# Kernel optimization log

Measured on AMD Instinct MI355X. Metric: run time of the kernel, lower is better.

The kernel has to match this reference:

```python
import jax, jax.numpy as jnp
import numpy as np

TAU = 0.2
NUM_SAMPLES = 8192
EMBED = 64


def setup_inputs() -> dict:
    key = jax.random.key(0)
    k1, k2, k3, k4 = jax.random.split(key, 4)
    all_users = jax.random.normal(k1, (100000, EMBED), dtype=jnp.float32)
    all_items = jax.random.normal(k2, (50000, EMBED), dtype=jnp.float32)
    user_index = jax.random.randint(k3, (NUM_SAMPLES,), 0, 100000, dtype=jnp.int64 if jax.config.jax_enable_x64 else jnp.int32)
    item_index = jax.random.randint(k4, (NUM_SAMPLES,), 0, 50000, dtype=jnp.int64 if jax.config.jax_enable_x64 else jnp.int32)
    return {"all_users": all_users, "all_items": all_items,
            "user_index": user_index, "item_index": item_index}


def _ssm_loss(embed, tau):
    # ratings: [N, N] similarity; positive is the diagonal (self-similarity).
    ratings = jnp.matmul(embed, embed.T) / tau            # [N, N]
    diag = jnp.sum(embed * embed, axis=1) / tau           # diag of embed@embed.T, no NxN gather
    # -log( exp(diag) / sum_j exp(ratings_ij) ) = logsumexp_row - diag
    lse = jax.scipy.special.logsumexp(ratings, axis=1)    # [N]
    return jnp.mean(lse - diag)


def reference(all_users, all_items, user_index, item_index):
    selected_users = all_users[user_index]                # [N, d]
    selected_items = all_items[item_index]                # [N, d]
    loss_u = _ssm_loss(selected_users, TAU)
    loss_i = _ssm_loss(selected_items, TAU)
    inv_loss = loss_u + loss_i
    return inv_loss, jnp.stack([loss_u, loss_i])
```

## Files before the change

kernel.cpp:

```cpp
#include <hip/hip_runtime.h>

#define EMBED        64
#define NS           8192
#define NTILE        256
#define JCHUNKS      8
#define JT_PER_CHUNK 32
#define C_L2E_TAU    7.21347520444482f

typedef _Float16 half8  __attribute__((ext_vector_type(8)));
typedef float    f32x16 __attribute__((ext_vector_type(16)));

static __device__ __forceinline__ float exp2_raw(float x) {
  float r;
  asm("v_exp_f32 %0, %1" : "=v"(r) : "v"(x));
  return r;
}

__global__ __launch_bounds__(256) void prep_kernel(
    const float* __restrict__ users, const float* __restrict__ items,
    const int* __restrict__ uidx, const int* __restrict__ iidx,
    _Float16* __restrict__ Efrag, float* __restrict__ diag) {
  int b = blockIdx.x;
  int mat = b >> 8, tile = b & 255;
  int kt = threadIdx.x >> 6;
  int lane = threadIdx.x & 63;
  int r = lane & 31;
  int k0 = kt * 16 + (lane >> 5) * 8;
  int row = tile * 32 + r;
  int src = mat ? iidx[row] : uidx[row];
  const float4* basep =
      (const float4*)((mat ? items : users) + (size_t)src * EMBED + k0);
  float4 v0 = basep[0], v1 = basep[1];
  float vs[8] = {v0.x, v0.y, v0.z, v0.w, v1.x, v1.y, v1.z, v1.w};

  half8 hh, ll;
  float p = 0.f;
  #pragma unroll
  for (int j = 0; j < 8; ++j) {
    float v = vs[j];
    _Float16 h = (_Float16)v;
    hh[j] = h;
    ll[j] = (_Float16)(v - (float)h);
    p = fmaf(v, v, p);
  }
  _Float16* tb = Efrag + (size_t)(mat * NTILE + tile) * 4096;
  *(half8*)(tb + ((kt)     * 64 + lane) * 8) = hh;
  *(half8*)(tb + ((4 + kt) * 64 + lane) * 8) = ll;

  p += __shfl_xor(p, 32);
  __shared__ float ds[4][32];
  if (lane < 32) ds[kt][lane] = p;
  __syncthreads();
  if (threadIdx.x < 32)
    diag[mat * NS + tile * 32 + threadIdx.x] =
        ds[0][threadIdx.x] + ds[1][threadIdx.x] +
        ds[2][threadIdx.x] + ds[3][threadIdx.x];
}

__global__ __launch_bounds__(256, 4) void ssm_mfma_kernel(
    const _Float16* __restrict__ Efrag, const float* __restrict__ diag,
    float* __restrict__ rowpart) {
  int b = blockIdx.x;
  int jc  = b & (JCHUNKS - 1);
  int sg  = (b >> 3) & 63;
  int mat = b >> 9;
  int wave = threadIdx.x >> 6;
  int lane = threadIdx.x & 63;
  int hf   = lane >> 5;

  int rowtile = sg * 4 + wave;
  const _Float16* Em = Efrag + (size_t)mat * NTILE * 4096;

  half8 a[8];
  #pragma unroll
  for (int f = 0; f < 8; ++f)
    a[f] = *(const half8*)(Em + (size_t)rowtile * 4096 + (f * 64 + lane) * 8);

  float negdv[16];
  #pragma unroll
  for (int r = 0; r < 16; ++r)
    negdv[r] = -diag[mat * NS + rowtile * 32 + (r & 3) + 8 * (r >> 2) + 4 * hf];

  float rs[16];
  #pragma unroll
  for (int r = 0; r < 16; ++r) rs[r] = 0.f;

  int tj0 = jc * JT_PER_CHUNK;

  #pragma unroll 2
  for (int jt = 0; jt < JT_PER_CHUNK; ++jt) {
    const _Float16* B = Em + (size_t)(tj0 + jt) * 4096;
    half8 bh[4], bl[4];
    #pragma unroll
    for (int k = 0; k < 4; ++k)
      bh[k] = *(const half8*)(B + ((k)     * 64 + lane) * 8);
    #pragma unroll
    for (int k = 0; k < 4; ++k)
      bl[k] = *(const half8*)(B + ((4 + k) * 64 + lane) * 8);

    f32x16 acc;
    #pragma unroll
    for (int r = 0; r < 16; ++r) acc[r] = negdv[r];

    #pragma unroll
    for (int k = 0; k < 4; ++k)
      acc = __builtin_amdgcn_mfma_f32_32x32x16_f16(a[k], bh[k], acc, 0, 0, 0);
    #pragma unroll
    for (int k = 0; k < 4; ++k)
      acc = __builtin_amdgcn_mfma_f32_32x32x16_f16(a[k], bl[k], acc, 0, 0, 0);
    #pragma unroll
    for (int k = 0; k < 4; ++k)
      acc = __builtin_amdgcn_mfma_f32_32x32x16_f16(a[4 + k], bh[k], acc, 0, 0, 0);

    #pragma unroll
    for (int r = 0; r < 16; ++r)
      rs[r] += exp2_raw(acc[r] * C_L2E_TAU);
  }

  #pragma unroll
  for (int r = 0; r < 16; ++r) {
    float v = rs[r];
    #pragma unroll
    for (int off = 16; off; off >>= 1) v += __shfl_xor(v, off);
    if ((lane & 31) == 0)
      rowpart[jc * (2 * NS) + mat * NS + rowtile * 32 +
              (r & 3) + 8 * (r >> 2) + 4 * hf] = v;
  }
}

__global__ __launch_bounds__(1024) void finalize_kernel(
    const float* __restrict__ rowpart, float* __restrict__ out) {
  float lu = 0.f, li = 0.f;
  for (int r = threadIdx.x; r < 2 * NS; r += 1024) {
    float s = 0.f;
    #pragma unroll
    for (int c = 0; c < JCHUNKS; ++c) s += rowpart[c * (2 * NS) + r];
    float l = logf(s);
    if (r < NS) lu += l; else li += l;
  }
  #pragma unroll
  for (int off = 32; off; off >>= 1) {
    lu += __shfl_down(lu, off);
    li += __shfl_down(li, off);
  }
  __shared__ float red[2][16];
  int wave = threadIdx.x >> 6;
  if ((threadIdx.x & 63) == 0) { red[0][wave] = lu; red[1][wave] = li; }
  __syncthreads();
  if (threadIdx.x == 0) {
    float su = 0.f, si = 0.f;
    #pragma unroll
    for (int w = 0; w < 16; ++w) { su += red[0][w]; si += red[1][w]; }
    su *= (1.0f / NS);
    si *= (1.0f / NS);
    out[0] = su + si;
    out[1] = su;
    out[2] = si;
  }
}

extern "C" void kernel_launch(void* const* d_in, const int* in_sizes, int n_in,
                              void* d_out, int out_size, void* d_ws, size_t ws_size,
                              hipStream_t stream) {
  const float* users = (const float*)d_in[0];
  const float* items = (const float*)d_in[1];
  const int*   uidx  = (const int*)d_in[2];
  const int*   iidx  = (const int*)d_in[3];
  float* out = (float*)d_out;

  _Float16* Efrag = (_Float16*)d_ws;
  float* diag     = (float*)((char*)d_ws + (size_t)4194304);
  float* rowpart  = diag + 2 * NS;

  prep_kernel<<<2 * NTILE, 256, 0, stream>>>(users, items, uidx, iidx, Efrag, diag);
  ssm_mfma_kernel<<<2 * 64 * JCHUNKS, 256, 0, stream>>>(Efrag, diag, rowpart);
  finalize_kernel<<<1, 1024, 0, stream>>>(rowpart, out);
}
```

Measured before the change: 146.3 us.

## Double-buffer B tile loads and split MFMA chain into independent accumulators

Restructures the j-loop into a software-pipelined double buffer, prefetching the next B tile into registers while the current tile runs through its MFMAs. The single dependent 12-MFMA chain becomes three independent accumulator chains that are summed afterwards, which shortens the dependency latency. The diagonal offset is pre-scaled and folded into a single fma before exp2. Launch bounds are relaxed from 4 to 2 blocks per CU to make room for the extra registers, which may lower occupancy.

```diff
diff --git a/kernel.cpp b/kernel.cpp
--- a/kernel.cpp
+++ b/kernel.cpp
@@ -57,7 +57,7 @@
         ds[2][threadIdx.x] + ds[3][threadIdx.x];
 }
 
-__global__ __launch_bounds__(256, 4) void ssm_mfma_kernel(
+__global__ __launch_bounds__(256, 2) void ssm_mfma_kernel(
     const _Float16* __restrict__ Efrag, const float* __restrict__ diag,
     float* __restrict__ rowpart) {
   int b = blockIdx.x;
@@ -76,10 +76,11 @@
   for (int f = 0; f < 8; ++f)
     a[f] = *(const half8*)(Em + (size_t)rowtile * 4096 + (f * 64 + lane) * 8);
 
-  float negdv[16];
+  float negdvC[16];
   #pragma unroll
   for (int r = 0; r < 16; ++r)
-    negdv[r] = -diag[mat * NS + rowtile * 32 + (r & 3) + 8 * (r >> 2) + 4 * hf];
+    negdvC[r] = -diag[mat * NS + rowtile * 32 +
+                      (r & 3) + 8 * (r >> 2) + 4 * hf] * C_L2E_TAU;
 
   float rs[16];
   #pragma unroll
@@ -87,34 +88,37 @@
 
   int tj0 = jc * JT_PER_CHUNK;
 
-  #pragma unroll 2
-  for (int jt = 0; jt < JT_PER_CHUNK; ++jt) {
-    const _Float16* B = Em + (size_t)(tj0 + jt) * 4096;
-    half8 bh[4], bl[4];
+  auto loadB = [&](int tj, half8* bb) {
+    const _Float16* B = Em + (size_t)tj * 4096;
     #pragma unroll
-    for (int k = 0; k < 4; ++k)
-      bh[k] = *(const half8*)(B + ((k)     * 64 + lane) * 8);
+    for (int f = 0; f < 8; ++f)
+      bb[f] = *(const half8*)(B + (f * 64 + lane) * 8);
+  };
+
+  auto compute = [&](const half8* bb) {
+    f32x16 c0 = {0.f,0.f,0.f,0.f,0.f,0.f,0.f,0.f,
+                 0.f,0.f,0.f,0.f,0.f,0.f,0.f,0.f};
+    f32x16 c1 = c0, c2 = c0;
     #pragma unroll
-    for (int k = 0; k < 4; ++k)
-      bl[k] = *(const half8*)(B + ((4 + k) * 64 + lane) * 8);
-
-    f32x16 acc;
-    #pragma unroll
-    for (int r = 0; r < 16; ++r) acc[r] = negdv[r];
-
-    #pragma unroll
-    for (int k = 0; k < 4; ++k)
-      acc = __builtin_amdgcn_mfma_f32_32x32x16_f16(a[k], bh[k], acc, 0, 0, 0);
-    #pragma unroll
-    for (int k = 0; k < 4; ++k)
-      acc = __builtin_amdgcn_mfma_f32_32x32x16_f16(a[k], bl[k], acc, 0, 0, 0);
-    #pragma unroll
-    for (int k = 0; k < 4; ++k)
-      acc = __builtin_amdgcn_mfma_f32_32x32x16_f16(a[4 + k], bh[k], acc, 0, 0, 0);
-
+    for (int k = 0; k < 4; ++k) {
+      c0 = __builtin_amdgcn_mfma_f32_32x32x16_f16(a[k],     bb[k],     c0, 0, 0, 0);
+      c1 = __builtin_amdgcn_mfma_f32_32x32x16_f16(a[k],     bb[4 + k], c1, 0, 0, 0);
+      c2 = __builtin_amdgcn_mfma_f32_32x32x16_f16(a[4 + k], bb[k],     c2, 0, 0, 0);
+    }
+    f32x16 s = (c0 + c1) + c2;
     #pragma unroll
     for (int r = 0; r < 16; ++r)
-      rs[r] += exp2_raw(acc[r] * C_L2E_TAU);
+      rs[r] += exp2_raw(fmaf(s[r], C_L2E_TAU, negdvC[r]));
+  };
+
+  half8 bA[8], bB[8];
+  loadB(tj0, bA);
+  #pragma unroll 1
+  for (int jt = 0; jt < JT_PER_CHUNK; jt += 2) {
+    loadB(tj0 + jt + 1, bB);
+    compute(bA);
+    if (jt + 2 < JT_PER_CHUNK) loadB(tj0 + jt + 2, bA);
+    compute(bB);
   }
 
   #pragma unroll
```

Result: no change. 148.6 us (+1.6%).

## Stage B tiles through LDS with async double-buffering and fuse finalize via atomic ticket

Applied to the files above, without the earlier changes.

The main kernel now copies pairs of B tiles into a double-buffered LDS area using global_load_lds, so the next pair loads while the current one is computed. All four waves in a block then share each B tile from LDS instead of each fetching it from global memory. The three MFMA chains now use separate accumulators so they can run independently. The separate finalize launch is removed: the last block to finish, picked by an atomic counter, does the log-sum reduction itself. This saves a kernel launch but adds block-wide syncs and 32 KB of LDS per block, which may reduce occupancy.

```diff
diff --git a/kernel.cpp b/kernel.cpp
--- a/kernel.cpp
+++ b/kernel.cpp
@@ -5,10 +5,16 @@
 #define NTILE        256
 #define JCHUNKS      8
 #define JT_PER_CHUNK 32
+#define NPHASE       (JT_PER_CHUNK / 2)
+#define NBLOCKS_MAIN (2 * 64 * JCHUNKS)
 #define C_L2E_TAU    7.21347520444482f
 
 typedef _Float16 half8  __attribute__((ext_vector_type(8)));
 typedef float    f32x16 __attribute__((ext_vector_type(16)));
+
+#define GLDS16(g, l) __builtin_amdgcn_global_load_lds( \
+    (const __attribute__((address_space(1))) void*)(g), \
+    (__attribute__((address_space(3))) void*)(l), 16, 0, 0)
 
 static __device__ __forceinline__ float exp2_raw(float x) {
   float r;
@@ -19,8 +25,10 @@
 __global__ __launch_bounds__(256) void prep_kernel(
     const float* __restrict__ users, const float* __restrict__ items,
     const int* __restrict__ uidx, const int* __restrict__ iidx,
-    _Float16* __restrict__ Efrag, float* __restrict__ diag) {
+    _Float16* __restrict__ Efrag, float* __restrict__ diag,
+    int* __restrict__ done_cnt) {
   int b = blockIdx.x;
+  if (b == 0 && threadIdx.x == 0) *done_cnt = 0;
   int mat = b >> 8, tile = b & 255;
   int kt = threadIdx.x >> 6;
   int lane = threadIdx.x & 63;
@@ -59,7 +67,8 @@
 
 __global__ __launch_bounds__(256, 4) void ssm_mfma_kernel(
     const _Float16* __restrict__ Efrag, const float* __restrict__ diag,
-    float* __restrict__ rowpart) {
+    float* __restrict__ rowpart, int* __restrict__ done_cnt,
+    float* __restrict__ out) {
   int b = blockIdx.x;
   int jc  = b & (JCHUNKS - 1);
   int sg  = (b >> 3) & 63;
@@ -85,36 +94,45 @@
   #pragma unroll
   for (int r = 0; r < 16; ++r) rs[r] = 0.f;
 
+  __shared__ __align__(16) _Float16 Bbuf[2][8192];
+
   int tj0 = jc * JT_PER_CHUNK;
-
-  #pragma unroll 2
-  for (int jt = 0; jt < JT_PER_CHUNK; ++jt) {
-    const _Float16* B = Em + (size_t)(tj0 + jt) * 4096;
-    half8 bh[4], bl[4];
-    #pragma unroll
-    for (int k = 0; k < 4; ++k)
-      bh[k] = *(const half8*)(B + ((k)     * 64 + lane) * 8);
-    #pragma unroll
-    for (int k = 0; k < 4; ++k)
-      bl[k] = *(const half8*)(B + ((4 + k) * 64 + lane) * 8);
-
-    f32x16 acc;
-    #pragma unroll
-    for (int r = 0; r < 16; ++r) acc[r] = negdv[r];
-
-    #pragma unroll
-    for (int k = 0; k < 4; ++k)
-      acc = __builtin_amdgcn_mfma_f32_32x32x16_f16(a[k], bh[k], acc, 0, 0, 0);
-    #pragma unroll
-    for (int k = 0; k < 4; ++k)
-      acc = __builtin_amdgcn_mfma_f32_32x32x16_f16(a[k], bl[k], acc, 0, 0, 0);
-    #pragma unroll
-    for (int k = 0; k < 4; ++k)
-      acc = __builtin_amdgcn_mfma_f32_32x32x16_f16(a[4 + k], bh[k], acc, 0, 0, 0);
-
+  auto stage = [&](int buf, int pair) {
+    const char* src = (const char*)(Em + (size_t)(tj0 + 2 * pair) * 4096);
+    char* dst = (char*)&Bbuf[buf][0];
+    int o = wave * 4096;
+    #pragma unroll
+    for (int q = 0; q < 4; ++q)
+      GLDS16(src + o + q * 1024 + lane * 16, dst + o + q * 1024);
+  };
+
+  auto compute = [&](const _Float16* B) {
+    f32x16 c0, c1, c2;
+    #pragma unroll
+    for (int r = 0; r < 16; ++r) { c0[r] = negdv[r]; c1[r] = 0.f; c2[r] = 0.f; }
+    #pragma unroll
+    for (int k = 0; k < 4; ++k) {
+      half8 bh = *(const half8*)(B + ((k)     * 64 + lane) * 8);
+      half8 bl = *(const half8*)(B + ((4 + k) * 64 + lane) * 8);
+      c0 = __builtin_amdgcn_mfma_f32_32x32x16_f16(a[k],     bh, c0, 0, 0, 0);
+      c1 = __builtin_amdgcn_mfma_f32_32x32x16_f16(a[k],     bl, c1, 0, 0, 0);
+      c2 = __builtin_amdgcn_mfma_f32_32x32x16_f16(a[4 + k], bh, c2, 0, 0, 0);
+    }
+    f32x16 s = (c0 + c1) + c2;
     #pragma unroll
     for (int r = 0; r < 16; ++r)
-      rs[r] += exp2_raw(acc[r] * C_L2E_TAU);
+      rs[r] += exp2_raw(s[r] * C_L2E_TAU);
+  };
+
+  stage(0, 0);
+  __syncthreads();
+
+  for (int p = 0; p < NPHASE; ++p) {
+    if (p + 1 < NPHASE) stage((p + 1) & 1, p + 1);
+    const _Float16* B = &Bbuf[p & 1][0];
+    compute(B);
+    compute(B + 4096);
+    __syncthreads();
   }
 
   #pragma unroll
@@ -126,36 +144,39 @@
       rowpart[jc * (2 * NS) + mat * NS + rowtile * 32 +
               (r & 3) + 8 * (r >> 2) + 4 * hf] = v;
   }
-}
-
-__global__ __launch_bounds__(1024) void finalize_kernel(
-    const float* __restrict__ rowpart, float* __restrict__ out) {
-  float lu = 0.f, li = 0.f;
-  for (int r = threadIdx.x; r < 2 * NS; r += 1024) {
-    float s = 0.f;
-    #pragma unroll
-    for (int c = 0; c < JCHUNKS; ++c) s += rowpart[c * (2 * NS) + r];
-    float l = logf(s);
-    if (r < NS) lu += l; else li += l;
-  }
-  #pragma unroll
-  for (int off = 32; off; off >>= 1) {
-    lu += __shfl_down(lu, off);
-    li += __shfl_down(li, off);
-  }
-  __shared__ float red[2][16];
-  int wave = threadIdx.x >> 6;
-  if ((threadIdx.x & 63) == 0) { red[0][wave] = lu; red[1][wave] = li; }
+
+  __shared__ int sticket;
+  __threadfence();
+  if (threadIdx.x == 0) sticket = atomicAdd(done_cnt, 1);
   __syncthreads();
-  if (threadIdx.x == 0) {
-    float su = 0.f, si = 0.f;
-    #pragma unroll
-    for (int w = 0; w < 16; ++w) { su += red[0][w]; si += red[1][w]; }
-    su *= (1.0f / NS);
-    si *= (1.0f / NS);
-    out[0] = su + si;
-    out[1] = su;
-    out[2] = si;
+  if (sticket == NBLOCKS_MAIN - 1) {
+    __threadfence();
+    float lu = 0.f, li = 0.f;
+    for (int r = threadIdx.x; r < 2 * NS; r += 256) {
+      float s = 0.f;
+      #pragma unroll
+      for (int c = 0; c < JCHUNKS; ++c) s += rowpart[c * (2 * NS) + r];
+      float l = logf(s);
+      if (r < NS) lu += l; else li += l;
+    }
+    #pragma unroll
+    for (int off = 32; off; off >>= 1) {
+      lu += __shfl_down(lu, off);
+      li += __shfl_down(li, off);
+    }
+    __shared__ float red[2][4];
+    if ((threadIdx.x & 63) == 0) {
+      red[0][threadIdx.x >> 6] = lu;
+      red[1][threadIdx.x >> 6] = li;
+    }
+    __syncthreads();
+    if (threadIdx.x == 0) {
+      float su = (red[0][0] + red[0][1] + red[0][2] + red[0][3]) * (1.0f / NS);
+      float si = (red[1][0] + red[1][1] + red[1][2] + red[1][3]) * (1.0f / NS);
+      out[0] = su + si;
+      out[1] = su;
+      out[2] = si;
+    }
   }
 }
 
@@ -171,8 +192,10 @@
   _Float16* Efrag = (_Float16*)d_ws;
   float* diag     = (float*)((char*)d_ws + (size_t)4194304);
   float* rowpart  = diag + 2 * NS;
-
-  prep_kernel<<<2 * NTILE, 256, 0, stream>>>(users, items, uidx, iidx, Efrag, diag);
-  ssm_mfma_kernel<<<2 * 64 * JCHUNKS, 256, 0, stream>>>(Efrag, diag, rowpart);
-  finalize_kernel<<<1, 1024, 0, stream>>>(rowpart, out);
-}
+  int* done_cnt   = (int*)(rowpart + JCHUNKS * 2 * NS);
+
+  prep_kernel<<<2 * NTILE, 256, 0, stream>>>(users, items, uidx, iidx,
+                                             Efrag, diag, done_cnt);
+  ssm_mfma_kernel<<<NBLOCKS_MAIN, 256, 0, stream>>>(Efrag, diag, rowpart,
+                                                    done_cnt, out);
+}
```

New measurement: 281.1 us. 92.2% more time.

## Exploit Gram matrix symmetry to compute only upper-triangle tiles with atomics

Applied to the files above, without the earlier changes.

Because embed@embed.T is symmetric, each 32x32 tile above the diagonal is now computed once. Its exp values are added both to the row sums and, through column sums and atomicAdd, to the transposed rows. This removes about half of the MFMA and exp work. B tiles are now staged into double-buffered LDS with global_load_lds, the grid is reorganised into 16 j-chunks with early exit for blocks below the diagonal, and per-chunk partial buffers are replaced by a single atomic accumulator zeroed in prep. The cost is more exp work per tile, atomic contention, load imbalance across blocks, and nondeterministic float summation order.

```diff
diff --git a/kernel.cpp b/kernel.cpp
--- a/kernel.cpp
+++ b/kernel.cpp
@@ -3,12 +3,16 @@
 #define EMBED        64
 #define NS           8192
 #define NTILE        256
-#define JCHUNKS      8
-#define JT_PER_CHUNK 32
+#define NJC          16
+#define JT_PER_CHUNK 16
 #define C_L2E_TAU    7.21347520444482f
 
 typedef _Float16 half8  __attribute__((ext_vector_type(8)));
 typedef float    f32x16 __attribute__((ext_vector_type(16)));
+
+#define GLDS16(g, l) __builtin_amdgcn_global_load_lds( \
+    (const __attribute__((address_space(1))) void*)(g), \
+    (__attribute__((address_space(3))) void*)(l), 16, 0, 0)
 
 static __device__ __forceinline__ float exp2_raw(float x) {
   float r;
@@ -19,9 +23,11 @@
 __global__ __launch_bounds__(256) void prep_kernel(
     const float* __restrict__ users, const float* __restrict__ items,
     const int* __restrict__ uidx, const int* __restrict__ iidx,
-    _Float16* __restrict__ Efrag, float* __restrict__ diag) {
+    _Float16* __restrict__ Efrag, float* __restrict__ diag,
+    float* __restrict__ accum) {
   int b = blockIdx.x;
   int mat = b >> 8, tile = b & 255;
+  if (threadIdx.x < 32) accum[mat * NS + tile * 32 + threadIdx.x] = 0.f;
   int kt = threadIdx.x >> 6;
   int lane = threadIdx.x & 63;
   int r = lane & 31;
@@ -57,64 +63,91 @@
         ds[2][threadIdx.x] + ds[3][threadIdx.x];
 }
 
-__global__ __launch_bounds__(256, 4) void ssm_mfma_kernel(
+__global__ __launch_bounds__(256) void ssm_mfma_kernel(
     const _Float16* __restrict__ Efrag, const float* __restrict__ diag,
-    float* __restrict__ rowpart) {
+    float* __restrict__ accum) {
   int b = blockIdx.x;
-  int jc  = b & (JCHUNKS - 1);
-  int sg  = (b >> 3) & 63;
-  int mat = b >> 9;
+  int jc  = b & (NJC - 1);
+  int ig  = (b >> 4) & 63;
+  int mat = b >> 10;
+  if (jc * 16 + 15 < ig * 4) return;
+
   int wave = threadIdx.x >> 6;
   int lane = threadIdx.x & 63;
   int hf   = lane >> 5;
-
-  int rowtile = sg * 4 + wave;
+  int myI  = ig * 4 + wave;
   const _Float16* Em = Efrag + (size_t)mat * NTILE * 4096;
 
   half8 a[8];
   #pragma unroll
   for (int f = 0; f < 8; ++f)
-    a[f] = *(const half8*)(Em + (size_t)rowtile * 4096 + (f * 64 + lane) * 8);
-
-  float negdv[16];
+    a[f] = *(const half8*)(Em + (size_t)myI * 4096 + (f * 64 + lane) * 8);
+
+  float negdIC[16];
   #pragma unroll
   for (int r = 0; r < 16; ++r)
-    negdv[r] = -diag[mat * NS + rowtile * 32 + (r & 3) + 8 * (r >> 2) + 4 * hf];
+    negdIC[r] = -diag[mat * NS + myI * 32 +
+                      (r & 3) + 8 * (r >> 2) + 4 * hf] * C_L2E_TAU;
 
   float rs[16];
   #pragma unroll
   for (int r = 0; r < 16; ++r) rs[r] = 0.f;
 
-  int tj0 = jc * JT_PER_CHUNK;
-
-  #pragma unroll 2
+  __shared__ __align__(16) _Float16 Bbuf[2][4096];
+
+  int J0 = jc * JT_PER_CHUNK;
+  auto stage = [&](int buf, int jt) {
+    const char* src = (const char*)(Em + (size_t)(J0 + jt) * 4096) + wave * 2048;
+    char* dst = (char*)&Bbuf[buf][0] + wave * 2048;
+    GLDS16(src + lane * 16, dst);
+    GLDS16(src + 1024 + lane * 16, dst + 1024);
+  };
+
+  stage(0, 0);
+  __syncthreads();
+
   for (int jt = 0; jt < JT_PER_CHUNK; ++jt) {
-    const _Float16* B = Em + (size_t)(tj0 + jt) * 4096;
-    half8 bh[4], bl[4];
-    #pragma unroll
-    for (int k = 0; k < 4; ++k)
-      bh[k] = *(const half8*)(B + ((k)     * 64 + lane) * 8);
-    #pragma unroll
-    for (int k = 0; k < 4; ++k)
-      bl[k] = *(const half8*)(B + ((4 + k) * 64 + lane) * 8);
-
-    f32x16 acc;
-    #pragma unroll
-    for (int r = 0; r < 16; ++r) acc[r] = negdv[r];
-
-    #pragma unroll
-    for (int k = 0; k < 4; ++k)
-      acc = __builtin_amdgcn_mfma_f32_32x32x16_f16(a[k], bh[k], acc, 0, 0, 0);
-    #pragma unroll
-    for (int k = 0; k < 4; ++k)
-      acc = __builtin_amdgcn_mfma_f32_32x32x16_f16(a[k], bl[k], acc, 0, 0, 0);
-    #pragma unroll
-    for (int k = 0; k < 4; ++k)
-      acc = __builtin_amdgcn_mfma_f32_32x32x16_f16(a[4 + k], bh[k], acc, 0, 0, 0);
-
-    #pragma unroll
-    for (int r = 0; r < 16; ++r)
-      rs[r] += exp2_raw(acc[r] * C_L2E_TAU);
+    int cur = jt & 1;
+    if (jt + 1 < JT_PER_CHUNK) stage(cur ^ 1, jt + 1);
+
+    int J = J0 + jt;
+    if (J >= myI) {
+      float negdJC = -diag[mat * NS + J * 32 + (lane & 31)] * C_L2E_TAU;
+
+      half8 bh[4], bl[4];
+      #pragma unroll
+      for (int k = 0; k < 4; ++k) {
+        bh[k] = *(const half8*)(&Bbuf[cur][0] + ((k)     * 64 + lane) * 8);
+        bl[k] = *(const half8*)(&Bbuf[cur][0] + ((4 + k) * 64 + lane) * 8);
+      }
+
+      f32x16 acc = {0.f,0.f,0.f,0.f,0.f,0.f,0.f,0.f,
+                    0.f,0.f,0.f,0.f,0.f,0.f,0.f,0.f};
+      #pragma unroll
+      for (int k = 0; k < 4; ++k)
+        acc = __builtin_amdgcn_mfma_f32_32x32x16_f16(a[k], bh[k], acc, 0, 0, 0);
+      #pragma unroll
+      for (int k = 0; k < 4; ++k)
+        acc = __builtin_amdgcn_mfma_f32_32x32x16_f16(a[k], bl[k], acc, 0, 0, 0);
+      #pragma unroll
+      for (int k = 0; k < 4; ++k)
+        acc = __builtin_amdgcn_mfma_f32_32x32x16_f16(a[4 + k], bh[k], acc, 0, 0, 0);
+
+      #pragma unroll
+      for (int r = 0; r < 16; ++r)
+        rs[r] += exp2_raw(fmaf(acc[r], C_L2E_TAU, negdIC[r]));
+
+      if (J > myI) {
+        float cs = 0.f;
+        #pragma unroll
+        for (int r = 0; r < 16; ++r)
+          cs += exp2_raw(fmaf(acc[r], C_L2E_TAU, negdJC));
+        cs += __shfl_xor(cs, 32);
+        if (lane < 32)
+          atomicAdd(&accum[mat * NS + J * 32 + lane], cs);
+      }
+    }
+    __syncthreads();
   }
 
   #pragma unroll
@@ -123,19 +156,16 @@
     #pragma unroll
     for (int off = 16; off; off >>= 1) v += __shfl_xor(v, off);
     if ((lane & 31) == 0)
-      rowpart[jc * (2 * NS) + mat * NS + rowtile * 32 +
-              (r & 3) + 8 * (r >> 2) + 4 * hf] = v;
+      atomicAdd(&accum[mat * NS + myI * 32 +
+                       (r & 3) + 8 * (r >> 2) + 4 * hf], v);
   }
 }
 
 __global__ __launch_bounds__(1024) void finalize_kernel(
-    const float* __restrict__ rowpart, float* __restrict__ out) {
+    const float* __restrict__ accum, float* __restrict__ out) {
   float lu = 0.f, li = 0.f;
   for (int r = threadIdx.x; r < 2 * NS; r += 1024) {
-    float s = 0.f;
-    #pragma unroll
-    for (int c = 0; c < JCHUNKS; ++c) s += rowpart[c * (2 * NS) + r];
-    float l = logf(s);
+    float l = logf(accum[r]);
     if (r < NS) lu += l; else li += l;
   }
   #pragma unroll
@@ -170,9 +200,10 @@
 
   _Float16* Efrag = (_Float16*)d_ws;
   float* diag     = (float*)((char*)d_ws + (size_t)4194304);
-  float* rowpart  = diag + 2 * NS;
-
-  prep_kernel<<<2 * NTILE, 256, 0, stream>>>(users, items, uidx, iidx, Efrag, diag);
-  ssm_mfma_kernel<<<2 * 64 * JCHUNKS, 256, 0, stream>>>(Efrag, diag, rowpart);
-  finalize_kernel<<<1, 1024, 0, stream>>>(rowpart, out);
-}
+  float* accum    = diag + 2 * NS;
+
+  prep_kernel<<<2 * NTILE, 256, 0, stream>>>(users, items, uidx, iidx,
+                                             Efrag, diag, accum);
+  ssm_mfma_kernel<<<2 * 64 * NJC, 256, 0, stream>>>(Efrag, diag, accum);
+  finalize_kernel<<<1, 1024, 0, stream>>>(accum, out);
+}
```

Measured after the change: 161.1 us. 1.1x slower.
